# Performance work log

Hardware: AMD Instinct MI355X
Metric: run time of the kernel (lower is better)

The kernel has to match this reference:

```python
import jax, jax.numpy as jnp
import numpy as np

N_NODES = 50000


def setup_inputs() -> dict:
    key = jax.random.key(0)
    k1, k2, k3, k4, k5, k6 = jax.random.split(key, 6)
    N, E, DIN, DOUT = N_NODES, 800000, 256, 256
    h = jax.random.normal(k1, (N, DIN), dtype=jnp.float32)
    e_w = jax.random.uniform(k2, (E, 1), dtype=jnp.float32)
    src = jax.random.randint(k3, (E,), 0, N, dtype=jnp.int32)
    dst = jax.random.randint(k4, (E,), 0, N, dtype=jnp.int32)
    stdv = 1.0 / np.sqrt(DOUT)
    weight = jax.random.uniform(k5, (DIN, DOUT), dtype=jnp.float32, minval=-stdv, maxval=stdv)
    bias = jax.random.uniform(k6, (DOUT,), dtype=jnp.float32, minval=-stdv, maxval=stdv)
    return {"h": h, "e_w": e_w, "src": src, "dst": dst, "weight": weight, "bias": bias}


def reference(h, e_w, src, dst, weight, bias):
    # u_mul_e: message m_e = h[src_e] * x_e  (edge weight broadcast over feature dim)
    m = h[src] * e_w                      # [E, DIN]
    # sum('m','h'): scatter-add messages to destination nodes
    agg = jax.ops.segment_sum(m, dst, num_segments=h.shape[0])  # [N, DIN]
    # dense GEMM + bias
    return agg @ weight + bias            # [N, DOUT]
```

## Files before the change

kernel.cpp:

```cpp
#include <hip/hip_runtime.h>
#include <hip/hip_bf16.h>


#define DIN 256
#define DOUT 256
#define CAP 64

typedef short bf16x8 __attribute__((ext_vector_type(8)));
typedef float f32x4  __attribute__((ext_vector_type(4)));
typedef unsigned short ushort8v __attribute__((ext_vector_type(8)));
typedef unsigned short ushort4v __attribute__((ext_vector_type(4)));

__device__ __forceinline__ unsigned short f2bf(float f) {
    unsigned u = __float_as_uint(f);
    u = (u + 0x7FFF + ((u >> 16) & 1)) >> 16;
    return (unsigned short)u;
}
__device__ __forceinline__ float bf2f(unsigned short s) {
    return __uint_as_float(((unsigned)s) << 16);
}

__global__ __launch_bounds__(256) void zero_int_kernel(int* __restrict__ p, int n) {
    int i = blockIdx.x * blockDim.x + threadIdx.x;
    int stride = gridDim.x * blockDim.x;
    for (; i < n; i += stride) p[i] = 0;
}

__global__ __launch_bounds__(256) void fill_kernel(const int* __restrict__ src,
                                                   const int* __restrict__ dst,
                                                   const float* __restrict__ e_w,
                                                   int* __restrict__ cursors,
                                                   int2* __restrict__ slots, int E) {
    int e = blockIdx.x * blockDim.x + threadIdx.x;
    if (e < E) {
        int d = dst[e];
        int pos = atomicAdd(&cursors[d], 1);
        if (pos < CAP)
            slots[(size_t)d * CAP + pos] = make_int2(src[e], __float_as_int(e_w[e]));
    }
}

__global__ __launch_bounds__(256) void wfrag_kernel(const float* __restrict__ W,
                                                    unsigned short* __restrict__ WTfrag) {
    int idx = blockIdx.x * 256 + threadIdx.x;
    if (idx >= 16 * 8 * 64) return;
    int lane = idx & 63;
    int tc = idx >> 6;
    int c = tc & 7;
    int t = tc >> 3;
    int q = lane >> 4, l16 = lane & 15;
    int col = t * 16 + l16;
    int krow = c * 32 + q * 8;
    ushort8v v;
#pragma unroll
    for (int j = 0; j < 8; ++j) v[j] = f2bf(W[(size_t)(krow + j) * DOUT + col]);
    *(ushort8v*)(WTfrag + (size_t)idx * 8) = v;
}

__global__ __launch_bounds__(256) void gemm_mfma_kernel(const float* __restrict__ h,
                                                        const unsigned short* __restrict__ WTfrag,
                                                        unsigned short* __restrict__ hW, int M) {
    __shared__ unsigned short Af[4 * 8 * 64 * 8];

    int tid = threadIdx.x;
    int block_row0 = blockIdx.x * 64;

#pragma unroll
    for (int j = 0; j < 16; ++j) {
        int flat = j * 256 + tid;
        int row  = flat >> 6;
        int col4 = (flat & 63) << 2;
        int r = block_row0 + row;
        float4 f = make_float4(0.f, 0.f, 0.f, 0.f);
        if (r < M) f = *(const float4*)(h + (size_t)r * DIN + col4);
        int w = row >> 4, l16r = row & 15;
        int c = col4 >> 5, q = (col4 >> 3) & 3, jj = col4 & 7;
        ushort4v u;
        u[0] = f2bf(f.x); u[1] = f2bf(f.y); u[2] = f2bf(f.z); u[3] = f2bf(f.w);
        *(ushort4v*)&Af[(size_t)(((w * 8 + c) * 64 + q * 16 + l16r) << 3) + jj] = u;
    }
    __syncthreads();

    int wave = tid >> 6;
    int lane = tid & 63;
    int quad = lane >> 4;
    int l16  = lane & 15;

    f32x4 acc[16];
#pragma unroll
    for (int t = 0; t < 16; ++t) acc[t] = (f32x4){0.f, 0.f, 0.f, 0.f};

#pragma unroll
    for (int c = 0; c < 8; ++c) {
        bf16x8 a = *(const bf16x8*)&Af[(size_t)(((wave * 8 + c) * 64 + lane)) * 8];
#pragma unroll
        for (int t = 0; t < 16; ++t) {
            bf16x8 b = *(const bf16x8*)(WTfrag + ((size_t)(t * 8 + c) * 64 + lane) * 8);
            acc[t] = __builtin_amdgcn_mfma_f32_16x16x32_bf16(a, b, acc[t], 0, 0, 0);
        }
    }

    int row0 = block_row0 + wave * 16;
#pragma unroll
    for (int t = 0; t < 16; ++t) {
#pragma unroll
        for (int r = 0; r < 4; ++r) {
            int row = row0 + quad * 4 + r;
            if (row < M)
                hW[(size_t)row * DOUT + t * 16 + l16] = f2bf(acc[t][r]);
        }
    }
}

__global__ __launch_bounds__(256) void gather_kernel(const unsigned short* __restrict__ hW,
                                                     const int2* __restrict__ slots,
                                                     const int* __restrict__ cursors,
                                                     const float* __restrict__ bias,
                                                     float* __restrict__ out, int N) {
    int node = blockIdx.x * 4 + (threadIdx.x >> 6);
    if (node >= N) return;
    int lane = threadIdx.x & 63;
    int half = lane >> 5;
    int l32  = lane & 31;
    int len  = cursors[node];
    if (len > CAP) len = CAP;
    const int2* sl = slots + (size_t)node * CAP;

    float acc[8] = {};
    int i = half;
    for (; i + 2 < len; i += 4) {
        int2 m0 = sl[i];
        int2 m1 = sl[i + 2];
        float w0 = __int_as_float(m0.y);
        float w1 = __int_as_float(m1.y);
        ushort8v v0 = *(const ushort8v*)(hW + (size_t)m0.x * DOUT + l32 * 8);
        ushort8v v1 = *(const ushort8v*)(hW + (size_t)m1.x * DOUT + l32 * 8);
#pragma unroll
        for (int j = 0; j < 8; ++j) acc[j] += w0 * bf2f(v0[j]) + w1 * bf2f(v1[j]);
    }
    if (i < len) {
        int2 m = sl[i];
        float w = __int_as_float(m.y);
        ushort8v v = *(const ushort8v*)(hW + (size_t)m.x * DOUT + l32 * 8);
#pragma unroll
        for (int j = 0; j < 8; ++j) acc[j] += w * bf2f(v[j]);
    }
#pragma unroll
    for (int j = 0; j < 8; ++j) acc[j] += __shfl_xor(acc[j], 32, 64);

    if (half == 0) {
        float4 b0 = *(const float4*)(bias + l32 * 8);
        float4 b1 = *(const float4*)(bias + l32 * 8 + 4);
        float* po = out + (size_t)node * DOUT + l32 * 8;
        *(float4*)po = make_float4(acc[0] + b0.x, acc[1] + b0.y, acc[2] + b0.z, acc[3] + b0.w);
        *((float4*)po + 1) = make_float4(acc[4] + b1.x, acc[5] + b1.y, acc[6] + b1.z, acc[7] + b1.w);
    }
}

extern "C" void kernel_launch(void* const* d_in, const int* in_sizes, int n_in,
                              void* d_out, int out_size, void* d_ws, size_t ws_size,
                              hipStream_t stream) {
    const float* h    = (const float*)d_in[0];
    const float* e_w  = (const float*)d_in[1];
    const int*   src  = (const int*)d_in[2];
    const int*   dst  = (const int*)d_in[3];
    const float* W    = (const float*)d_in[4];
    const float* bias = (const float*)d_in[5];
    float* out = (float*)d_out;

    int N = in_sizes[0] / DIN;
    int E = in_sizes[1];

    char* base = (char*)d_ws;
    unsigned short* WTfrag = (unsigned short*)base;
    size_t off = (size_t)DIN * DOUT * sizeof(unsigned short);
    unsigned short* hW = (unsigned short*)(base + off);
    off += (size_t)N * DOUT * sizeof(unsigned short);
    int* cursors = (int*)(base + off);
    off += (size_t)N * sizeof(int);
    off = (off + 15) & ~(size_t)15;
    int2* slots = (int2*)(base + off);
    off += (size_t)N * CAP * sizeof(int2);

    zero_int_kernel<<<128, 256, 0, stream>>>(cursors, N);
    fill_kernel<<<(E + 255) / 256, 256, 0, stream>>>(src, dst, e_w, cursors, slots, E);
    wfrag_kernel<<<32, 256, 0, stream>>>(W, WTfrag);
    gemm_mfma_kernel<<<(N + 63) / 64, 256, 0, stream>>>(h, WTfrag, hW, N);
    gather_kernel<<<(N + 3) / 4, 256, 0, stream>>>(hW, slots, cursors, bias, out, N);
}
```

Before: 248.8 us.

## Persistent GEMM with register-resident weights, fused prep kernel, per-lane gather

Merges weight-fragment conversion and cursor zeroing into one prep kernel, removing a launch. The GEMM becomes persistent with 512 blocks. Each wave keeps its quarter of the weight fragments in registers and loops over 64-row tiles, avoiding repeated global weight loads, at the cost of higher register pressure. The gather kernel drops the half-wave split and cross-lane shuffle: each lane handles 4 columns and consumes 4 edges per iteration, which gives smaller per-lane loads but more edge-slot reads per lane.

```diff
diff --git a/kernel.cpp b/kernel.cpp
--- a/kernel.cpp
+++ b/kernel.cpp
@@ -20,10 +20,24 @@
     return __uint_as_float(((unsigned)s) << 16);
 }
 
-__global__ __launch_bounds__(256) void zero_int_kernel(int* __restrict__ p, int n) {
-    int i = blockIdx.x * blockDim.x + threadIdx.x;
-    int stride = gridDim.x * blockDim.x;
-    for (; i < n; i += stride) p[i] = 0;
+__global__ __launch_bounds__(256) void prep_kernel(const float* __restrict__ W,
+                                                   unsigned short* __restrict__ WTfrag,
+                                                   int* __restrict__ cursors, int N) {
+    int gid = blockIdx.x * 256 + threadIdx.x;
+    if (gid < 16 * 8 * 64) {
+        int lane = gid & 63;
+        int tc = gid >> 6;
+        int c = tc & 7;
+        int t = tc >> 3;
+        int q = lane >> 4, l16 = lane & 15;
+        int col = t * 16 + l16;
+        int krow = c * 32 + q * 8;
+        ushort8v v;
+#pragma unroll
+        for (int j = 0; j < 8; ++j) v[j] = f2bf(W[(size_t)(krow + j) * DOUT + col]);
+        *(ushort8v*)(WTfrag + (size_t)gid * 8) = v;
+    }
+    for (int i = gid; i < N; i += gridDim.x * 256) cursors[i] = 0;
 }
 
 __global__ __launch_bounds__(256) void fill_kernel(const int* __restrict__ src,
@@ -40,74 +54,67 @@
     }
 }
 
-__global__ __launch_bounds__(256) void wfrag_kernel(const float* __restrict__ W,
-                                                    unsigned short* __restrict__ WTfrag) {
-    int idx = blockIdx.x * 256 + threadIdx.x;
-    if (idx >= 16 * 8 * 64) return;
-    int lane = idx & 63;
-    int tc = idx >> 6;
-    int c = tc & 7;
-    int t = tc >> 3;
-    int q = lane >> 4, l16 = lane & 15;
-    int col = t * 16 + l16;
-    int krow = c * 32 + q * 8;
-    ushort8v v;
-#pragma unroll
-    for (int j = 0; j < 8; ++j) v[j] = f2bf(W[(size_t)(krow + j) * DOUT + col]);
-    *(ushort8v*)(WTfrag + (size_t)idx * 8) = v;
-}
-
-__global__ __launch_bounds__(256) void gemm_mfma_kernel(const float* __restrict__ h,
-                                                        const unsigned short* __restrict__ WTfrag,
-                                                        unsigned short* __restrict__ hW, int M) {
+__global__ __launch_bounds__(256, 2) void gemm_mfma_kernel(const float* __restrict__ h,
+                                                           const unsigned short* __restrict__ WTfrag,
+                                                           unsigned short* __restrict__ hW,
+                                                           int M, int ntiles) {
     __shared__ unsigned short Af[4 * 8 * 64 * 8];
 
-    int tid = threadIdx.x;
-    int block_row0 = blockIdx.x * 64;
-
-#pragma unroll
-    for (int j = 0; j < 16; ++j) {
-        int flat = j * 256 + tid;
-        int row  = flat >> 6;
-        int col4 = (flat & 63) << 2;
-        int r = block_row0 + row;
-        float4 f = make_float4(0.f, 0.f, 0.f, 0.f);
-        if (r < M) f = *(const float4*)(h + (size_t)r * DIN + col4);
-        int w = row >> 4, l16r = row & 15;
-        int c = col4 >> 5, q = (col4 >> 3) & 3, jj = col4 & 7;
-        ushort4v u;
-        u[0] = f2bf(f.x); u[1] = f2bf(f.y); u[2] = f2bf(f.z); u[3] = f2bf(f.w);
-        *(ushort4v*)&Af[(size_t)(((w * 8 + c) * 64 + q * 16 + l16r) << 3) + jj] = u;
-    }
-    __syncthreads();
-
+    int tid  = threadIdx.x;
     int wave = tid >> 6;
     int lane = tid & 63;
     int quad = lane >> 4;
     int l16  = lane & 15;
 
-    f32x4 acc[16];
+    bf16x8 breg[4][8];
 #pragma unroll
-    for (int t = 0; t < 16; ++t) acc[t] = (f32x4){0.f, 0.f, 0.f, 0.f};
+    for (int tq = 0; tq < 4; ++tq)
+#pragma unroll
+        for (int c = 0; c < 8; ++c)
+            breg[tq][c] = *(const bf16x8*)(WTfrag +
+                ((size_t)((wave * 4 + tq) * 8 + c) * 64 + lane) * 8);
+
+    for (int tile = blockIdx.x; tile < ntiles; tile += gridDim.x) {
+        int row0 = tile * 64;
+        __syncthreads();
+#pragma unroll
+        for (int j = 0; j < 16; ++j) {
+            int flat = j * 256 + tid;
+            int row  = flat >> 6;
+            int col4 = (flat & 63) << 2;
+            int r = row0 + row;
+            float4 f = make_float4(0.f, 0.f, 0.f, 0.f);
+            if (r < M) f = *(const float4*)(h + (size_t)r * DIN + col4);
+            int w = row >> 4, l16r = row & 15;
+            int c = col4 >> 5, q = (col4 >> 3) & 3, jj = col4 & 7;
+            ushort4v u;
+            u[0] = f2bf(f.x); u[1] = f2bf(f.y); u[2] = f2bf(f.z); u[3] = f2bf(f.w);
+            *(ushort4v*)&Af[(size_t)(((w * 8 + c) * 64 + q * 16 + l16r) << 3) + jj] = u;
+        }
+        __syncthreads();
 
 #pragma unroll
-    for (int c = 0; c < 8; ++c) {
-        bf16x8 a = *(const bf16x8*)&Af[(size_t)(((wave * 8 + c) * 64 + lane)) * 8];
+        for (int s = 0; s < 4; ++s) {
+            f32x4 acc[4];
 #pragma unroll
-        for (int t = 0; t < 16; ++t) {
-            bf16x8 b = *(const bf16x8*)(WTfrag + ((size_t)(t * 8 + c) * 64 + lane) * 8);
-            acc[t] = __builtin_amdgcn_mfma_f32_16x16x32_bf16(a, b, acc[t], 0, 0, 0);
-        }
-    }
-
-    int row0 = block_row0 + wave * 16;
+            for (int tq = 0; tq < 4; ++tq) acc[tq] = (f32x4){0.f, 0.f, 0.f, 0.f};
 #pragma unroll
-    for (int t = 0; t < 16; ++t) {
+            for (int c = 0; c < 8; ++c) {
+                bf16x8 a = *(const bf16x8*)&Af[(size_t)((s * 8 + c) * 64 + lane) * 8];
 #pragma unroll
-        for (int r = 0; r < 4; ++r) {
-            int row = row0 + quad * 4 + r;
-            if (row < M)
-                hW[(size_t)row * DOUT + t * 16 + l16] = f2bf(acc[t][r]);
+                for (int tq = 0; tq < 4; ++tq)
+                    acc[tq] = __builtin_amdgcn_mfma_f32_16x16x32_bf16(a, breg[tq][c], acc[tq], 0, 0, 0);
+            }
+            int r0 = row0 + s * 16;
+#pragma unroll
+            for (int tq = 0; tq < 4; ++tq) {
+#pragma unroll
+                for (int r = 0; r < 4; ++r) {
+                    int row = r0 + quad * 4 + r;
+                    if (row < M)
+                        hW[(size_t)row * DOUT + (wave * 4 + tq) * 16 + l16] = f2bf(acc[tq][r]);
+                }
+            }
         }
     }
 }
@@ -120,41 +127,37 @@
     int node = blockIdx.x * 4 + (threadIdx.x >> 6);
     if (node >= N) return;
     int lane = threadIdx.x & 63;
-    int half = lane >> 5;
-    int l32  = lane & 31;
     int len  = cursors[node];
     if (len > CAP) len = CAP;
     const int2* sl = slots + (size_t)node * CAP;
 
-    float acc[8] = {};
-    int i = half;
-    for (; i + 2 < len; i += 4) {
-        int2 m0 = sl[i];
-        int2 m1 = sl[i + 2];
-        float w0 = __int_as_float(m0.y);
-        float w1 = __int_as_float(m1.y);
-        ushort8v v0 = *(const ushort8v*)(hW + (size_t)m0.x * DOUT + l32 * 8);
-        ushort8v v1 = *(const ushort8v*)(hW + (size_t)m1.x * DOUT + l32 * 8);
-#pragma unroll
-        for (int j = 0; j < 8; ++j) acc[j] += w0 * bf2f(v0[j]) + w1 * bf2f(v1[j]);
+    float a0 = 0.f, a1 = 0.f, a2 = 0.f, a3 = 0.f;
+    int i = 0;
+    for (; i + 4 <= len; i += 4) {
+        int2 m0 = sl[i], m1 = sl[i + 1], m2 = sl[i + 2], m3 = sl[i + 3];
+        float w0 = __int_as_float(m0.y), w1 = __int_as_float(m1.y);
+        float w2 = __int_as_float(m2.y), w3 = __int_as_float(m3.y);
+        ushort4v v0 = *(const ushort4v*)(hW + (size_t)m0.x * DOUT + lane * 4);
+        ushort4v v1 = *(const ushort4v*)(hW + (size_t)m1.x * DOUT + lane * 4);
+        ushort4v v2 = *(const ushort4v*)(hW + (size_t)m2.x * DOUT + lane * 4);
+        ushort4v v3 = *(const ushort4v*)(hW + (size_t)m3.x * DOUT + lane * 4);
+        a0 += w0 * bf2f(v0[0]) + w1 * bf2f(v1[0]) + w2 * bf2f(v2[0]) + w3 * bf2f(v3[0]);
+        a1 += w0 * bf2f(v0[1]) + w1 * bf2f(v1[1]) + w2 * bf2f(v2[1]) + w3 * bf2f(v3[1]);
+        a2 += w0 * bf2f(v0[2]) + w1 * bf2f(v1[2]) + w2 * bf2f(v2[2]) + w3 * bf2f(v3[2]);
+        a3 += w0 * bf2f(v0[3]) + w1 * bf2f(v1[3]) + w2 * bf2f(v2[3]) + w3 * bf2f(v3[3]);
     }
-    if (i < len) {
+    for (; i < len; ++i) {
         int2 m = sl[i];
         float w = __int_as_float(m.y);
-        ushort8v v = *(const ushort8v*)(hW + (size_t)m.x * DOUT + l32 * 8);
-#pragma unroll
-        for (int j = 0; j < 8; ++j) acc[j] += w * bf2f(v[j]);
+        ushort4v v = *(const ushort4v*)(hW + (size_t)m.x * DOUT + lane * 4);
+        a0 += w * bf2f(v[0]);
+        a1 += w * bf2f(v[1]);
+        a2 += w * bf2f(v[2]);
+        a3 += w * bf2f(v[3]);
     }
-#pragma unroll
-    for (int j = 0; j < 8; ++j) acc[j] += __shfl_xor(acc[j], 32, 64);
-
-    if (half == 0) {
-        float4 b0 = *(const float4*)(bias + l32 * 8);
-        float4 b1 = *(const float4*)(bias + l32 * 8 + 4);
-        float* po = out + (size_t)node * DOUT + l32 * 8;
-        *(float4*)po = make_float4(acc[0] + b0.x, acc[1] + b0.y, acc[2] + b0.z, acc[3] + b0.w);
-        *((float4*)po + 1) = make_float4(acc[4] + b1.x, acc[5] + b1.y, acc[6] + b1.z, acc[7] + b1.w);
-    }
+    float4 b = *(const float4*)(bias + lane * 4);
+    *(float4*)(out + (size_t)node * DOUT + lane * 4) =
+        make_float4(a0 + b.x, a1 + b.y, a2 + b.z, a3 + b.w);
 }
 
 extern "C" void kernel_launch(void* const* d_in, const int* in_sizes, int n_in,
@@ -170,6 +173,7 @@
 
     int N = in_sizes[0] / DIN;
     int E = in_sizes[1];
+    int ntiles = (N + 63) / 64;
 
     char* base = (char*)d_ws;
     unsigned short* WTfrag = (unsigned short*)base;
@@ -182,9 +186,8 @@
     int2* slots = (int2*)(base + off);
     off += (size_t)N * CAP * sizeof(int2);
 
-    zero_int_kernel<<<128, 256, 0, stream>>>(cursors, N);
+    prep_kernel<<<64, 256, 0, stream>>>(W, WTfrag, cursors, N);
     fill_kernel<<<(E + 255) / 256, 256, 0, stream>>>(src, dst, e_w, cursors, slots, E);
-    wfrag_kernel<<<32, 256, 0, stream>>>(W, WTfrag);
-    gemm_mfma_kernel<<<(N + 63) / 64, 256, 0, stream>>>(h, WTfrag, hW, N);
+    gemm_mfma_kernel<<<512, 256, 0, stream>>>(h, WTfrag, hW, N, ntiles);
     gather_kernel<<<(N + 3) / 4, 256, 0, stream>>>(hW, slots, cursors, bias, out, N);
 }
```

Measured after the change: 233.3 us. 6.3% less time.
